# Performance work log

Hardware: AMD Instinct MI355X
Metric: run time of the kernel (lower is better)

The kernel has to match this reference:

```python
import jax, jax.numpy as jnp
import numpy as np

AT_ID = 5       # tokenizer id of '@'
CITSEG_ID = 7   # tokenizer id of 'CITSEG'


def setup_inputs() -> dict:
    key = jax.random.key(0)
    ks = jax.random.split(key, 12)
    B, S, H = 256, 512, 768
    CIT, D, NC = 750, 1518, 6
    s = lambda n: 1.0 / np.sqrt(n)
    return {
        "tokens": jax.random.randint(ks[0], (B, S), 0, 100),
        "hidden_states": jax.random.normal(ks[1], (B, S, H), jnp.float32),
        "proj_w": jax.random.normal(ks[2], (H, CIT), jnp.float32) * s(H),
        "proj_b": jax.random.normal(ks[3], (CIT,), jnp.float32) * 0.02,
        "enc_w": jax.random.normal(ks[4], (CIT, CIT), jnp.float32) * s(CIT),
        "enc_b": jax.random.normal(ks[5], (CIT,), jnp.float32) * 0.02,
        "w1": jax.random.normal(ks[6], (D, 2 * D), jnp.float32) * s(D),
        "b1": jax.random.normal(ks[7], (2 * D,), jnp.float32) * 0.02,
        "w2": jax.random.normal(ks[8], (2 * D, 2 * D), jnp.float32) * s(2 * D),
        "b2": jax.random.normal(ks[9], (2 * D,), jnp.float32) * 0.02,
        "w3": jax.random.normal(ks[10], (2 * D, NC), jnp.float32) * s(2 * D),
        "b3": jax.random.normal(ks[11], (NC,), jnp.float32) * 0.02,
    }


def _forward(tokens, hidden_states, proj_w, proj_b, enc_w, enc_b,
             w1, b1, w2, b2, w3, b3):
    B, S, H = hidden_states.shape
    idx = jnp.arange(S)[None, :]                       # [1,S]
    BIG = S + 1

    # --- ctx_pooler: masked max over tokens outside the [start,end] '@' span ---
    at_mask = tokens == AT_ID                          # [B,S]
    first = jnp.min(jnp.where(at_mask, idx, BIG), axis=1)            # [B]
    second = jnp.min(jnp.where(at_mask & (idx > first[:, None]), idx, BIG), axis=1)
    ge2 = at_mask.sum(axis=1) >= 2
    start = jnp.where(ge2, first, 0)
    end = jnp.where(ge2, second, S)                    # end=S excludes everything
    keep = (idx < start[:, None]) | (idx > end[:, None])             # [B,S]
    neg = jnp.finfo(hidden_states.dtype).min
    pooled = jnp.max(jnp.where(keep[:, :, None], hidden_states, neg), axis=1)  # [B,H]
    pooled = jnp.where(keep.any(axis=1)[:, None], pooled, 0.0)

    # --- CITSEG token gather + projection (zero row if absent) ---
    c_mask = tokens == CITSEG_ID
    c_first = jnp.min(jnp.where(c_mask, idx, BIG), axis=1)           # [B]
    has_c = c_mask.any(axis=1)
    safe_pos = jnp.minimum(c_first, S - 1)
    cit_h = jnp.take_along_axis(hidden_states, safe_pos[:, None, None], axis=1)[:, 0]  # [B,H]
    cit = (cit_h @ proj_w + proj_b) * has_c[:, None].astype(hidden_states.dtype)       # [B,750]

    # --- citseg_encoder (modeled as Linear 750->750) ---
    cit_enc = cit @ enc_w + enc_b

    # --- MLP head ---
    x = jnp.concatenate([pooled, cit_enc], axis=1)     # [B,1518]
    x = jax.nn.relu(x @ w1 + b1)
    x = jax.nn.relu(x @ w2 + b2)
    return x @ w3 + b3                                 # [B,num_class]


def reference(tokens, hidden_states, proj_w, proj_b, enc_w, enc_b,
              w1, b1, w2, b2, w3, b3):
    return _forward(tokens, hidden_states, proj_w, proj_b, enc_w, enc_b,
                    w1, b1, w2, b2, w3, b3)
```

## Files before the change

### kernel.cpp

```cpp
#include <hip/hip_runtime.h>
#include <hip/hip_bf16.h>

typedef __attribute__((ext_vector_type(8))) short bf16x8;
typedef __attribute__((ext_vector_type(4))) float f32x4;
typedef __attribute__((ext_vector_type(4))) unsigned short u16x4;

#define NEGINF (-3.4028234663852886e38f)

__device__ __forceinline__ unsigned short f2b(float f) {
    union { float f; unsigned u; } x; x.f = f;
    unsigned r = x.u + 0x7FFFu + ((x.u >> 16) & 1u);
    return (unsigned short)(r >> 16);
}
__device__ __forceinline__ float b2f(unsigned short b) {
    union { unsigned u; float f; } x; x.u = ((unsigned)b) << 16;
    return x.f;
}

__device__ __forceinline__ void load_lds16(const void* g, void* l) {
    __builtin_amdgcn_global_load_lds((const __attribute__((address_space(1))) void*)g,
                                     (__attribute__((address_space(3))) void*)l, 16, 0, 0);
}

__device__ __forceinline__ void trans32(const float* __restrict__ in, int K, int N,
                                        unsigned short* __restrict__ out, int ldo,
                                        int bx, int by, int tid, float (*tile)[33]) {
    int n0 = bx * 32, k0 = by * 32;
    int tx = tid & 31, ty = tid >> 5;
#pragma unroll
    for (int i = 0; i < 4; ++i) {
        int k = k0 + ty * 4 + i, n = n0 + tx;
        tile[ty * 4 + i][tx] = (k < K && n < N) ? in[(size_t)k * N + n] : 0.f;
    }
    __syncthreads();
    int n = tid >> 3, kc = tid & 7;
    u16x4 o;
#pragma unroll
    for (int q = 0; q < 4; ++q) o[q] = f2b(tile[kc * 4 + q][n]);
    *(u16x4*)(out + (size_t)(n0 + n) * ldo + k0 + kc * 4) = o;
}

__global__ __launch_bounds__(256) void prep_k(
    const int* __restrict__ tokens, int* __restrict__ meta,
    const float* __restrict__ proj_w, const float* __restrict__ enc_w,
    const float* __restrict__ w1, const float* __restrict__ w2,
    unsigned short* __restrict__ projT, unsigned short* __restrict__ encT,
    unsigned short* __restrict__ w1T, unsigned short* __restrict__ w2T) {
    __shared__ float tile[32][33];
    int bid = blockIdx.x, tid = threadIdx.x;
    if (bid < 64) {
        const int S = 512, BIG = 1 << 20;
        int b = bid * 4 + (tid >> 6), l = tid & 63;
        const int* row = tokens + (size_t)b * S;
        int base = l * 8;
        int toks[8];
#pragma unroll
        for (int i = 0; i < 8; ++i) toks[i] = row[base + i];
        int am = 0, cnt = 0, minAt = BIG, minC = BIG;
#pragma unroll
        for (int i = 0; i < 8; ++i) {
            if (toks[i] == 5) { am |= 1 << i; cnt++; if (base + i < minAt) minAt = base + i; }
            if (toks[i] == 7) { if (base + i < minC) minC = base + i; }
        }
        for (int off = 1; off < 64; off <<= 1) {
            minAt = min(minAt, __shfl_xor(minAt, off));
            minC  = min(minC,  __shfl_xor(minC,  off));
            cnt  += __shfl_xor(cnt, off);
        }
        int first = minAt, minAt2 = BIG;
#pragma unroll
        for (int i = 0; i < 8; ++i)
            if ((am >> i) & 1) { int idx = base + i; if (idx > first && idx < minAt2) minAt2 = idx; }
        for (int off = 1; off < 64; off <<= 1) minAt2 = min(minAt2, __shfl_xor(minAt2, off));
        if (l == 0) {
            int ge2 = (cnt >= 2) ? 1 : 0;
            int start = ge2 ? first : 0;
            int end = ge2 ? minAt2 : S;
            int anyKeep = (ge2 && (start > 0 || end < S - 1)) ? 1 : 0;
            int has_c = (minC < S) ? 1 : 0;
            int cpos = min(minC, S - 1);
            int* m = meta + b * 6;
            m[0] = start; m[1] = end; m[2] = cpos; m[3] = has_c; m[4] = anyKeep; m[5] = 0;
        }
    } else if (bid < 640) {
        int r = bid - 64;   trans32(proj_w, 768, 750, projT, 768, r % 24, r / 24, tid, tile);
    } else if (bid < 1216) {
        int r = bid - 640;  trans32(enc_w, 750, 750, encT, 768, r % 24, r / 24, tid, tile);
    } else if (bid < 5824) {
        int r = bid - 1216; trans32(w1, 1518, 3036, w1T, 1536, r % 96, r / 96, tid, tile);
    } else {
        int r = bid - 5824; trans32(w2, 3036, 3036, w2T, 3072, r % 96, r / 96, tid, tile);
    }
}

__global__ __launch_bounds__(192) void pool_k(const float* __restrict__ hs,
                                              const int* __restrict__ meta,
                                              float* __restrict__ part) {
    int b = blockIdx.x >> 3, ch = blockIdx.x & 7;
    int start = meta[b * 6 + 0], end = meta[b * 6 + 1];
    int t = threadIdx.x;
    f32x4 m = { NEGINF, NEGINF, NEGINF, NEGINF };
    const float* basep = hs + (size_t)b * 512 * 768 + t * 4;
    int s0 = ch * 64, hi = s0 + 64;
    int e1 = min(start, hi);
    int s2 = max(end + 1, s0);
#pragma unroll 4
    for (int s = s0; s < e1; ++s) {
        f32x4 v = *(const f32x4*)(basep + (size_t)s * 768);
#pragma unroll
        for (int j = 0; j < 4; ++j) m[j] = fmaxf(m[j], v[j]);
    }
#pragma unroll 4
    for (int s = s2; s < hi; ++s) {
        f32x4 v = *(const f32x4*)(basep + (size_t)s * 768);
#pragma unroll
        for (int j = 0; j < 4; ++j) m[j] = fmaxf(m[j], v[j]);
    }
    *(f32x4*)(part + ((size_t)b * 8 + ch) * 768 + t * 4) = m;
}

__global__ __launch_bounds__(192) void pack_k(const float* __restrict__ hs,
                                              const float* __restrict__ part,
                                              const int* __restrict__ meta,
                                              unsigned short* __restrict__ xA,
                                              unsigned short* __restrict__ citA) {
    int b = blockIdx.x, t = threadIdx.x;
    const float* p = part + (size_t)b * 8 * 768 + t * 4;
    f32x4 m = *(const f32x4*)p;
#pragma unroll
    for (int ch = 1; ch < 8; ++ch) {
        f32x4 v = *(const f32x4*)(p + (size_t)ch * 768);
#pragma unroll
        for (int j = 0; j < 4; ++j) m[j] = fmaxf(m[j], v[j]);
    }
    if (!meta[b * 6 + 4]) {
        f32x4 z = {0.f, 0.f, 0.f, 0.f};
        m = z;
    }
    u16x4 o;
#pragma unroll
    for (int j = 0; j < 4; ++j) o[j] = f2b(m[j]);
    *(u16x4*)(xA + (size_t)b * 1536 + t * 4) = o;

    int cpos = meta[b * 6 + 2];
    f32x4 c = *(const f32x4*)(hs + ((size_t)b * 512 + cpos) * 768 + t * 4);
    u16x4 co;
#pragma unroll
    for (int j = 0; j < 4; ++j) co[j] = f2b(c[j]);
    *(u16x4*)(citA + (size_t)b * 768 + t * 4) = co;
}

template<int EPI>
__global__ __launch_bounds__(256, 2) void gemm_k(
    const unsigned short* __restrict__ A, int lda,
    const unsigned short* __restrict__ Bt, int ldb,
    const float* __restrict__ bias, const int* __restrict__ meta,
    unsigned short* __restrict__ X, int ldx, int Nreal, int Kp) {
    __shared__ __align__(16) unsigned short As[2][64 * 128];
    __shared__ __align__(16) unsigned short Bs[2][64 * 128];
    const int tid = threadIdx.x;
    const int wid = tid >> 6, lane = tid & 63;
    const int m0 = blockIdx.y * 64, n0 = blockIdx.x * 64;
    const int wr = wid >> 1, wc = wid & 1;
    const int c_lin = lane & 15;
    const int rsub = lane >> 4;

    int aoff[4], boff[4], ldst[4];
#pragma unroll
    for (int i = 0; i < 4; ++i) {
        int r = wid * 16 + i * 4 + rsub;
        int csrc = (c_lin ^ (r & 15)) << 3;
        aoff[i] = (m0 + r) * lda + csrc;
        boff[i] = (n0 + r) * ldb + csrc;
        ldst[i] = (wid * 16 + i * 4) * 128;
    }
    int cswz[4];
#pragma unroll
    for (int ks = 0; ks < 4; ++ks) cswz[ks] = ((ks * 4 + (lane >> 4)) ^ c_lin) << 3;
    int arow[2], brow[2];
#pragma unroll
    for (int mi = 0; mi < 2; ++mi) arow[mi] = (wr * 32 + mi * 16 + c_lin) * 128;
#pragma unroll
    for (int nj = 0; nj < 2; ++nj) brow[nj] = (wc * 32 + nj * 16 + c_lin) * 128;

    f32x4 acc[2][2];
    const f32x4 zero = {0.f, 0.f, 0.f, 0.f};
#pragma unroll
    for (int mi = 0; mi < 2; ++mi)
#pragma unroll
        for (int nj = 0; nj < 2; ++nj) acc[mi][nj] = zero;

    auto stage = [&](int nb, int kt) {
#pragma unroll
        for (int i = 0; i < 4; ++i) load_lds16(A + aoff[i] + kt, &As[nb][ldst[i]]);
#pragma unroll
        for (int i = 0; i < 4; ++i) load_lds16(Bt + boff[i] + kt, &Bs[nb][ldst[i]]);
    };

    const int nt = Kp >> 7;
    stage(0, 0);
    int cb = 0;
    for (int t = 0; t < nt; ++t) {
        __syncthreads();
        if (t + 1 < nt) stage(cb ^ 1, (t + 1) << 7);
        const unsigned short* as = As[cb];
        const unsigned short* bs = Bs[cb];
#pragma unroll
        for (int ks = 0; ks < 4; ++ks) {
            bf16x8 af[2], bfr[2];
#pragma unroll
            for (int mi = 0; mi < 2; ++mi) af[mi] = *(const bf16x8*)(as + arow[mi] + cswz[ks]);
#pragma unroll
            for (int nj = 0; nj < 2; ++nj) bfr[nj] = *(const bf16x8*)(bs + brow[nj] + cswz[ks]);
#pragma unroll
            for (int mi = 0; mi < 2; ++mi)
#pragma unroll
                for (int nj = 0; nj < 2; ++nj)
                    acc[mi][nj] = __builtin_amdgcn_mfma_f32_16x16x32_bf16(
                        af[mi], bfr[nj], acc[mi][nj], 0, 0, 0);
        }
        cb ^= 1;
    }
#pragma unroll
    for (int mi = 0; mi < 2; ++mi) {
        int rowb = m0 + wr * 32 + mi * 16 + (lane >> 4) * 4;
#pragma unroll
        for (int nj = 0; nj < 2; ++nj) {
            int col = n0 + wc * 32 + nj * 16 + (lane & 15);
            float bv = (col < Nreal) ? bias[col] : 0.f;
#pragma unroll
            for (int i = 0; i < 4; ++i) {
                int row = rowb + i;
                float v = acc[mi][nj][i] + bv;
                if (EPI == 0) v *= (meta[row * 6 + 3] ? 1.f : 0.f);
                if (EPI == 2) v = fmaxf(v, 0.f);
                if (col >= Nreal) v = 0.f;
                X[(size_t)row * ldx + col] = f2b(v);
            }
        }
    }
}

__global__ __launch_bounds__(256) void out_k(const unsigned short* __restrict__ x2,
                                             const float* __restrict__ w3,
                                             const float* __restrict__ b3,
                                             float* __restrict__ out) {
    int b = blockIdx.x, t = threadIdx.x;
    int wid = t >> 6, lane = t & 63;
    float s[6] = {0.f, 0.f, 0.f, 0.f, 0.f, 0.f};
    const unsigned short* xr = x2 + (size_t)b * 3072;
    for (int k = t; k < 3036; k += 256) {
        float x = b2f(xr[k]);
#pragma unroll
        for (int j = 0; j < 6; ++j) s[j] += x * w3[(size_t)k * 6 + j];
    }
#pragma unroll
    for (int j = 0; j < 6; ++j)
        for (int off = 1; off < 64; off <<= 1) s[j] += __shfl_xor(s[j], off);
    __shared__ float red[4][6];
    if (lane == 0) {
#pragma unroll
        for (int j = 0; j < 6; ++j) red[wid][j] = s[j];
    }
    __syncthreads();
    if (t < 6) out[b * 6 + t] = red[0][t] + red[1][t] + red[2][t] + red[3][t] + b3[t];
}

extern "C" void kernel_launch(void* const* d_in, const int* in_sizes, int n_in,
                              void* d_out, int out_size, void* d_ws, size_t ws_size,
                              hipStream_t stream) {
    const int*   tokens = (const int*)d_in[0];
    const float* hs     = (const float*)d_in[1];
    const float* proj_w = (const float*)d_in[2];
    const float* proj_b = (const float*)d_in[3];
    const float* enc_w  = (const float*)d_in[4];
    const float* enc_b  = (const float*)d_in[5];
    const float* w1 = (const float*)d_in[6];
    const float* b1 = (const float*)d_in[7];
    const float* w2 = (const float*)d_in[8];
    const float* b2 = (const float*)d_in[9];
    const float* w3 = (const float*)d_in[10];
    const float* b3 = (const float*)d_in[11];
    float* out = (float*)d_out;

    char* ws = (char*)d_ws;
    size_t off = 0;
    auto alloc = [&](size_t bytes) {
        void* p = ws + off;
        off = (off + bytes + 255) & ~(size_t)255;
        return p;
    };
    int* meta            = (int*)alloc(256 * 6 * sizeof(int));
    float* part          = (float*)alloc((size_t)256 * 8 * 768 * sizeof(float));
    unsigned short* xA   = (unsigned short*)alloc((size_t)256 * 1536 * 2);
    unsigned short* citA = (unsigned short*)alloc((size_t)256 * 768 * 2);
    unsigned short* citB = (unsigned short*)alloc((size_t)256 * 768 * 2);
    unsigned short* x1   = (unsigned short*)alloc((size_t)256 * 3072 * 2);
    unsigned short* x2   = (unsigned short*)alloc((size_t)256 * 3072 * 2);
    unsigned short* projT= (unsigned short*)alloc((size_t)768 * 768 * 2);
    unsigned short* encT = (unsigned short*)alloc((size_t)768 * 768 * 2);
    unsigned short* w1T  = (unsigned short*)alloc((size_t)3072 * 1536 * 2);
    unsigned short* w2T  = (unsigned short*)alloc((size_t)3072 * 3072 * 2);

    prep_k<<<15040, 256, 0, stream>>>(tokens, meta, proj_w, enc_w, w1, w2,
                                      projT, encT, w1T, w2T);
    pool_k<<<2048, 192, 0, stream>>>(hs, meta, part);
    pack_k<<<256, 192, 0, stream>>>(hs, part, meta, xA, citA);

    gemm_k<0><<<dim3(12, 4), 256, 0, stream>>>(citA, 768, projT, 768, proj_b, meta,
                                               citB, 768, 750, 768);
    gemm_k<1><<<dim3(12, 4), 256, 0, stream>>>(citB, 768, encT, 768, enc_b, meta,
                                               xA + 768, 1536, 750, 768);
    gemm_k<2><<<dim3(48, 4), 256, 0, stream>>>(xA, 1536, w1T, 1536, b1, meta,
                                               x1, 3072, 3036, 1536);
    gemm_k<2><<<dim3(48, 4), 256, 0, stream>>>(x1, 3072, w2T, 3072, b2, meta,
                                               x2, 3072, 3036, 3072);
    out_k<<<256, 256, 0, stream>>>(x2, w3, b3, out);
}
```

Baseline: 165.9 us.

## Fuse pooling with weight transposes and pack with first GEMM into fewer launches

```diff
diff --git a/kernel.cpp b/kernel.cpp
--- a/kernel.cpp
+++ b/kernel.cpp
@@ -16,41 +16,20 @@
     union { unsigned u; float f; } x; x.u = ((unsigned)b) << 16;
     return x.f;
 }
-
 __device__ __forceinline__ void load_lds16(const void* g, void* l) {
     __builtin_amdgcn_global_load_lds((const __attribute__((address_space(1))) void*)g,
                                      (__attribute__((address_space(3))) void*)l, 16, 0, 0);
 }
 
-__device__ __forceinline__ void trans32(const float* __restrict__ in, int K, int N,
-                                        unsigned short* __restrict__ out, int ldo,
-                                        int bx, int by, int tid, float (*tile)[33]) {
-    int n0 = bx * 32, k0 = by * 32;
-    int tx = tid & 31, ty = tid >> 5;
-#pragma unroll
-    for (int i = 0; i < 4; ++i) {
-        int k = k0 + ty * 4 + i, n = n0 + tx;
-        tile[ty * 4 + i][tx] = (k < K && n < N) ? in[(size_t)k * N + n] : 0.f;
-    }
-    __syncthreads();
-    int n = tid >> 3, kc = tid & 7;
-    u16x4 o;
-#pragma unroll
-    for (int q = 0; q < 4; ++q) o[q] = f2b(tile[kc * 4 + q][n]);
-    *(u16x4*)(out + (size_t)(n0 + n) * ldo + k0 + kc * 4) = o;
-}
-
-__global__ __launch_bounds__(256) void prep_k(
-    const int* __restrict__ tokens, int* __restrict__ meta,
-    const float* __restrict__ proj_w, const float* __restrict__ enc_w,
-    const float* __restrict__ w1, const float* __restrict__ w2,
-    unsigned short* __restrict__ projT, unsigned short* __restrict__ encT,
-    unsigned short* __restrict__ w1T, unsigned short* __restrict__ w2T) {
-    __shared__ float tile[32][33];
-    int bid = blockIdx.x, tid = threadIdx.x;
-    if (bid < 64) {
-        const int S = 512, BIG = 1 << 20;
-        int b = bid * 4 + (tid >> 6), l = tid & 63;
+__global__ __launch_bounds__(192) void scan_cit_k(const int* __restrict__ tokens,
+                                                  const float* __restrict__ hs,
+                                                  int* __restrict__ meta,
+                                                  unsigned short* __restrict__ citA) {
+    __shared__ int sm;
+    const int S = 512, BIG = 1 << 20;
+    int b = blockIdx.x, tid = threadIdx.x;
+    if (tid < 64) {
+        int l = tid;
         const int* row = tokens + (size_t)b * S;
         int base = l * 8;
         int toks[8];
@@ -81,73 +60,201 @@
             int cpos = min(minC, S - 1);
             int* m = meta + b * 6;
             m[0] = start; m[1] = end; m[2] = cpos; m[3] = has_c; m[4] = anyKeep; m[5] = 0;
-        }
-    } else if (bid < 640) {
-        int r = bid - 64;   trans32(proj_w, 768, 750, projT, 768, r % 24, r / 24, tid, tile);
-    } else if (bid < 1216) {
-        int r = bid - 640;  trans32(enc_w, 750, 750, encT, 768, r % 24, r / 24, tid, tile);
-    } else if (bid < 5824) {
-        int r = bid - 1216; trans32(w1, 1518, 3036, w1T, 1536, r % 96, r / 96, tid, tile);
-    } else {
-        int r = bid - 5824; trans32(w2, 3036, 3036, w2T, 3072, r % 96, r / 96, tid, tile);
-    }
-}
-
-__global__ __launch_bounds__(192) void pool_k(const float* __restrict__ hs,
-                                              const int* __restrict__ meta,
-                                              float* __restrict__ part) {
-    int b = blockIdx.x >> 3, ch = blockIdx.x & 7;
-    int start = meta[b * 6 + 0], end = meta[b * 6 + 1];
-    int t = threadIdx.x;
-    f32x4 m = { NEGINF, NEGINF, NEGINF, NEGINF };
-    const float* basep = hs + (size_t)b * 512 * 768 + t * 4;
-    int s0 = ch * 64, hi = s0 + 64;
-    int e1 = min(start, hi);
-    int s2 = max(end + 1, s0);
+            sm = cpos;
+        }
+    }
+    __syncthreads();
+    int cpos = sm;
+    f32x4 c = *(const f32x4*)(hs + ((size_t)b * 512 + cpos) * 768 + tid * 4);
+    u16x4 co;
+#pragma unroll
+    for (int j = 0; j < 4; ++j) co[j] = f2b(c[j]);
+    *(u16x4*)(citA + (size_t)b * 768 + tid * 4) = co;
+}
+
+__device__ __forceinline__ void trans32(const float* __restrict__ in, int K, int N,
+                                        unsigned short* __restrict__ out, int ldo,
+                                        int bx, int by, int tid, float (*tile)[33]) {
+    int n0 = bx * 32, k0 = by * 32;
+    int tx = tid & 31, ty = tid >> 5;
+#pragma unroll
+    for (int i = 0; i < 4; ++i) {
+        int k = k0 + ty * 4 + i, n = n0 + tx;
+        tile[ty * 4 + i][tx] = (k < K && n < N) ? in[(size_t)k * N + n] : 0.f;
+    }
+    __syncthreads();
+    int n = tid >> 3, kc = tid & 7;
+    u16x4 o;
+#pragma unroll
+    for (int q = 0; q < 4; ++q) o[q] = f2b(tile[kc * 4 + q][n]);
+    *(u16x4*)(out + (size_t)(n0 + n) * ldo + k0 + kc * 4) = o;
+}
+
+__global__ __launch_bounds__(256) void pool_trans_k(
+    const float* __restrict__ hs, const int* __restrict__ meta,
+    float* __restrict__ part,
+    const float* __restrict__ proj_w, const float* __restrict__ enc_w,
+    const float* __restrict__ w1, const float* __restrict__ w2,
+    unsigned short* __restrict__ projT, unsigned short* __restrict__ encT,
+    unsigned short* __restrict__ w1T, unsigned short* __restrict__ w2T) {
+    __shared__ float tile[32][33];
+    int bid = blockIdx.x, tid = threadIdx.x;
+    if (bid < 2048) {
+        if (tid >= 192) return;
+        int b = bid >> 3, ch = bid & 7;
+        int start = meta[b * 6 + 0], end = meta[b * 6 + 1];
+        f32x4 m = { NEGINF, NEGINF, NEGINF, NEGINF };
+        const float* basep = hs + (size_t)b * 512 * 768 + tid * 4;
+        int s0 = ch * 64, hi = s0 + 64;
+        int e1 = min(start, hi);
+        int s2 = max(end + 1, s0);
 #pragma unroll 4
-    for (int s = s0; s < e1; ++s) {
-        f32x4 v = *(const f32x4*)(basep + (size_t)s * 768);
-#pragma unroll
-        for (int j = 0; j < 4; ++j) m[j] = fmaxf(m[j], v[j]);
-    }
+        for (int s = s0; s < e1; ++s) {
+            f32x4 v = *(const f32x4*)(basep + (size_t)s * 768);
+#pragma unroll
+            for (int j = 0; j < 4; ++j) m[j] = fmaxf(m[j], v[j]);
+        }
 #pragma unroll 4
-    for (int s = s2; s < hi; ++s) {
-        f32x4 v = *(const f32x4*)(basep + (size_t)s * 768);
-#pragma unroll
-        for (int j = 0; j < 4; ++j) m[j] = fmaxf(m[j], v[j]);
-    }
-    *(f32x4*)(part + ((size_t)b * 8 + ch) * 768 + t * 4) = m;
-}
-
-__global__ __launch_bounds__(192) void pack_k(const float* __restrict__ hs,
-                                              const float* __restrict__ part,
-                                              const int* __restrict__ meta,
-                                              unsigned short* __restrict__ xA,
-                                              unsigned short* __restrict__ citA) {
-    int b = blockIdx.x, t = threadIdx.x;
-    const float* p = part + (size_t)b * 8 * 768 + t * 4;
-    f32x4 m = *(const f32x4*)p;
-#pragma unroll
-    for (int ch = 1; ch < 8; ++ch) {
-        f32x4 v = *(const f32x4*)(p + (size_t)ch * 768);
-#pragma unroll
-        for (int j = 0; j < 4; ++j) m[j] = fmaxf(m[j], v[j]);
-    }
-    if (!meta[b * 6 + 4]) {
-        f32x4 z = {0.f, 0.f, 0.f, 0.f};
-        m = z;
-    }
-    u16x4 o;
-#pragma unroll
-    for (int j = 0; j < 4; ++j) o[j] = f2b(m[j]);
-    *(u16x4*)(xA + (size_t)b * 1536 + t * 4) = o;
-
-    int cpos = meta[b * 6 + 2];
-    f32x4 c = *(const f32x4*)(hs + ((size_t)b * 512 + cpos) * 768 + t * 4);
-    u16x4 co;
-#pragma unroll
-    for (int j = 0; j < 4; ++j) co[j] = f2b(c[j]);
-    *(u16x4*)(citA + (size_t)b * 768 + t * 4) = co;
+        for (int s = s2; s < hi; ++s) {
+            f32x4 v = *(const f32x4*)(basep + (size_t)s * 768);
+#pragma unroll
+            for (int j = 0; j < 4; ++j) m[j] = fmaxf(m[j], v[j]);
+        }
+        *(f32x4*)(part + ((size_t)b * 8 + ch) * 768 + tid * 4) = m;
+        return;
+    }
+    int r = bid - 2048;
+    if (r < 576)       { trans32(proj_w, 768, 750, projT, 768, r % 24, r / 24, tid, tile); return; }
+    r -= 576;
+    if (r < 576)       { trans32(enc_w, 750, 750, encT, 768, r % 24, r / 24, tid, tile); return; }
+    r -= 576;
+    if (r < 4608)      { trans32(w1, 1518, 3036, w1T, 1536, r % 96, r / 96, tid, tile); return; }
+    r -= 4608;
+    trans32(w2, 3036, 3036, w2T, 3072, r % 96, r / 96, tid, tile);
+}
+
+template<int EPI>
+__device__ __forceinline__ void gemm_body(
+    const unsigned short* __restrict__ A, int lda,
+    const unsigned short* __restrict__ Bt, int ldb,
+    const float* __restrict__ bias, const int* __restrict__ meta,
+    unsigned short* __restrict__ X, int ldx, int Nreal, int Kp,
+    int bx, int by, unsigned short* AsB, unsigned short* BsB) {
+    const int tid = threadIdx.x;
+    const int wid = tid >> 6, lane = tid & 63;
+    const int m0 = by * 64, n0 = bx * 64;
+    const int wr = wid >> 1, wc = wid & 1;
+    const int c_lin = lane & 15;
+    const int rsub = lane >> 4;
+
+    int aoff[4], boff[4], ldst[4];
+#pragma unroll
+    for (int i = 0; i < 4; ++i) {
+        int r = wid * 16 + i * 4 + rsub;
+        int csrc = (c_lin ^ (r & 15)) << 3;
+        aoff[i] = (m0 + r) * lda + csrc;
+        boff[i] = (n0 + r) * ldb + csrc;
+        ldst[i] = (wid * 16 + i * 4) * 128;
+    }
+    int cswz[4];
+#pragma unroll
+    for (int ks = 0; ks < 4; ++ks) cswz[ks] = ((ks * 4 + (lane >> 4)) ^ c_lin) << 3;
+    int arow[2], brow[2];
+#pragma unroll
+    for (int mi = 0; mi < 2; ++mi) arow[mi] = (wr * 32 + mi * 16 + c_lin) * 128;
+#pragma unroll
+    for (int nj = 0; nj < 2; ++nj) brow[nj] = (wc * 32 + nj * 16 + c_lin) * 128;
+
+    f32x4 acc[2][2];
+    const f32x4 zero = {0.f, 0.f, 0.f, 0.f};
+#pragma unroll
+    for (int mi = 0; mi < 2; ++mi)
+#pragma unroll
+        for (int nj = 0; nj < 2; ++nj) acc[mi][nj] = zero;
+
+    auto stage = [&](int nb, int kt) {
+#pragma unroll
+        for (int i = 0; i < 4; ++i) load_lds16(A + aoff[i] + kt, AsB + nb * 8192 + ldst[i]);
+#pragma unroll
+        for (int i = 0; i < 4; ++i) load_lds16(Bt + boff[i] + kt, BsB + nb * 8192 + ldst[i]);
+    };
+
+    const int nt = Kp >> 7;
+    stage(0, 0);
+    int cb = 0;
+    for (int t = 0; t < nt; ++t) {
+        __syncthreads();
+        if (t + 1 < nt) stage(cb ^ 1, (t + 1) << 7);
+        const unsigned short* as = AsB + cb * 8192;
+        const unsigned short* bs = BsB + cb * 8192;
+#pragma unroll
+        for (int ks = 0; ks < 4; ++ks) {
+            bf16x8 af[2], bfr[2];
+#pragma unroll
+            for (int mi = 0; mi < 2; ++mi) af[mi] = *(const bf16x8*)(as + arow[mi] + cswz[ks]);
+#pragma unroll
+            for (int nj = 0; nj < 2; ++nj) bfr[nj] = *(const bf16x8*)(bs + brow[nj] + cswz[ks]);
+#pragma unroll
+            for (int mi = 0; mi < 2; ++mi)
+#pragma unroll
+                for (int nj = 0; nj < 2; ++nj)
+                    acc[mi][nj] = __builtin_amdgcn_mfma_f32_16x16x32_bf16(
+                        af[mi], bfr[nj], acc[mi][nj], 0, 0, 0);
+        }
+        cb ^= 1;
+    }
+#pragma unroll
+    for (int mi = 0; mi < 2; ++mi) {
+        int rowb = m0 + wr * 32 + mi * 16 + (lane >> 4) * 4;
+#pragma unroll
+        for (int nj = 0; nj < 2; ++nj) {
+            int col = n0 + wc * 32 + nj * 16 + (lane & 15);
+            float bv = (col < Nreal) ? bias[col] : 0.f;
+#pragma unroll
+            for (int i = 0; i < 4; ++i) {
+                int row = rowb + i;
+                float v = acc[mi][nj][i] + bv;
+                if (EPI == 0) v *= (meta[row * 6 + 3] ? 1.f : 0.f);
+                if (EPI == 2) v = fmaxf(v, 0.f);
+                if (col >= Nreal) v = 0.f;
+                X[(size_t)row * ldx + col] = f2b(v);
+            }
+        }
+    }
+}
+
+__global__ __launch_bounds__(256, 2) void pack_g1_k(
+    const float* __restrict__ part, const int* __restrict__ meta,
+    unsigned short* __restrict__ xA,
+    const unsigned short* __restrict__ citA, const unsigned short* __restrict__ projT,
+    const float* __restrict__ proj_b, unsigned short* __restrict__ citB) {
+    __shared__ __align__(16) unsigned short As[2][64 * 128];
+    __shared__ __align__(16) unsigned short Bs[2][64 * 128];
+    int bid = blockIdx.x, tid = threadIdx.x;
+    if (bid < 256) {
+        if (tid >= 192) return;
+        int b = bid;
+        const float* p = part + (size_t)b * 8 * 768 + tid * 4;
+        f32x4 m = *(const f32x4*)p;
+#pragma unroll
+        for (int ch = 1; ch < 8; ++ch) {
+            f32x4 v = *(const f32x4*)(p + (size_t)ch * 768);
+#pragma unroll
+            for (int j = 0; j < 4; ++j) m[j] = fmaxf(m[j], v[j]);
+        }
+        if (!meta[b * 6 + 4]) {
+            f32x4 z = {0.f, 0.f, 0.f, 0.f};
+            m = z;
+        }
+        u16x4 o;
+#pragma unroll
+        for (int j = 0; j < 4; ++j) o[j] = f2b(m[j]);
+        *(u16x4*)(xA + (size_t)b * 1536 + tid * 4) = o;
+        return;
+    }
+    int r = bid - 256;
+    gemm_body<0>(citA, 768, projT, 768, proj_b, meta, citB, 768, 750, 768,
+                 r % 12, r / 12, &As[0][0], &Bs[0][0]);
 }
 
 template<int EPI>
@@ -158,87 +265,8 @@
     unsigned short* __restrict__ X, int ldx, int Nreal, int Kp) {
     __shared__ __align__(16) unsigned short As[2][64 * 128];
     __shared__ __align__(16) unsigned short Bs[2][64 * 128];
-    const int tid = threadIdx.x;
-    const int wid = tid >> 6, lane = tid & 63;
-    const int m0 = blockIdx.y * 64, n0 = blockIdx.x * 64;
-    const int wr = wid >> 1, wc = wid & 1;
-    const int c_lin = lane & 15;
-    const int rsub = lane >> 4;
-
-    int aoff[4], boff[4], ldst[4];
-#pragma unroll
-    for (int i = 0; i < 4; ++i) {
-        int r = wid * 16 + i * 4 + rsub;
-        int csrc = (c_lin ^ (r & 15)) << 3;
-        aoff[i] = (m0 + r) * lda + csrc;
-        boff[i] = (n0 + r) * ldb + csrc;
-        ldst[i] = (wid * 16 + i * 4) * 128;
-    }
-    int cswz[4];
-#pragma unroll
-    for (int ks = 0; ks < 4; ++ks) cswz[ks] = ((ks * 4 + (lane >> 4)) ^ c_lin) << 3;
-    int arow[2], brow[2];
-#pragma unroll
-    for (int mi = 0; mi < 2; ++mi) arow[mi] = (wr * 32 + mi * 16 + c_lin) * 128;
-#pragma unroll
-    for (int nj = 0; nj < 2; ++nj) brow[nj] = (wc * 32 + nj * 16 + c_lin) * 128;
-
-    f32x4 acc[2][2];
-    const f32x4 zero = {0.f, 0.f, 0.f, 0.f};
-#pragma unroll
-    for (int mi = 0; mi < 2; ++mi)
-#pragma unroll
-        for (int nj = 0; nj < 2; ++nj) acc[mi][nj] = zero;
-
-    auto stage = [&](int nb, int kt) {
-#pragma unroll
-        for (int i = 0; i < 4; ++i) load_lds16(A + aoff[i] + kt, &As[nb][ldst[i]]);
-#pragma unroll
-        for (int i = 0; i < 4; ++i) load_lds16(Bt + boff[i] + kt, &Bs[nb][ldst[i]]);
-    };
-
-    const int nt = Kp >> 7;
-    stage(0, 0);
-    int cb = 0;
-    for (int t = 0; t < nt; ++t) {
-        __syncthreads();
-        if (t + 1 < nt) stage(cb ^ 1, (t + 1) << 7);
-        const unsigned short* as = As[cb];
-        const unsigned short* bs = Bs[cb];
-#pragma unroll
-        for (int ks = 0; ks < 4; ++ks) {
-            bf16x8 af[2], bfr[2];
-#pragma unroll
-            for (int mi = 0; mi < 2; ++mi) af[mi] = *(const bf16x8*)(as + arow[mi] + cswz[ks]);
-#pragma unroll
-            for (int nj = 0; nj < 2; ++nj) bfr[nj] = *(const bf16x8*)(bs + brow[nj] + cswz[ks]);
-#pragma unroll
-            for (int mi = 0; mi < 2; ++mi)
-#pragma unroll
-                for (int nj = 0; nj < 2; ++nj)
-                    acc[mi][nj] = __builtin_amdgcn_mfma_f32_16x16x32_bf16(
-                        af[mi], bfr[nj], acc[mi][nj], 0, 0, 0);
-        }
-        cb ^= 1;
-    }
-#pragma unroll
-    for (int mi = 0; mi < 2; ++mi) {
-        int rowb = m0 + wr * 32 + mi * 16 + (lane >> 4) * 4;
-#pragma unroll
-        for (int nj = 0; nj < 2; ++nj) {
-            int col = n0 + wc * 32 + nj * 16 + (lane & 15);
-            float bv = (col < Nreal) ? bias[col] : 0.f;
-#pragma unroll
-            for (int i = 0; i < 4; ++i) {
-                int row = rowb + i;
-                float v = acc[mi][nj][i] + bv;
-                if (EPI == 0) v *= (meta[row * 6 + 3] ? 1.f : 0.f);
-                if (EPI == 2) v = fmaxf(v, 0.f);
-                if (col >= Nreal) v = 0.f;
-                X[(size_t)row * ldx + col] = f2b(v);
-            }
-        }
-    }
+    gemm_body<EPI>(A, lda, Bt, ldb, bias, meta, X, ldx, Nreal, Kp,
+                   blockIdx.x, blockIdx.y, &As[0][0], &Bs[0][0]);
 }
 
 __global__ __launch_bounds__(256) void out_k(const unsigned short* __restrict__ x2,
@@ -302,13 +330,10 @@
     unsigned short* w1T  = (unsigned short*)alloc((size_t)3072 * 1536 * 2);
     unsigned short* w2T  = (unsigned short*)alloc((size_t)3072 * 3072 * 2);
 
-    prep_k<<<15040, 256, 0, stream>>>(tokens, meta, proj_w, enc_w, w1, w2,
-                                      projT, encT, w1T, w2T);
-    pool_k<<<2048, 192, 0, stream>>>(hs, meta, part);
-    pack_k<<<256, 192, 0, stream>>>(hs, part, meta, xA, citA);
-
-    gemm_k<0><<<dim3(12, 4), 256, 0, stream>>>(citA, 768, projT, 768, proj_b, meta,
-                                               citB, 768, 750, 768);
+    scan_cit_k<<<256, 192, 0, stream>>>(tokens, hs, meta, citA);
+    pool_trans_k<<<2048 + 576 + 576 + 4608 + 9216, 256, 0, stream>>>(
+        hs, meta, part, proj_w, enc_w, w1, w2, projT, encT, w1T, w2T);
+    pack_g1_k<<<304, 256, 0, stream>>>(part, meta, xA, citA, projT, proj_b, citB);
     gemm_k<1><<<dim3(12, 4), 256, 0, stream>>>(citB, 768, encT, 768, enc_b, meta,
                                                xA + 768, 1536, 750, 768);
     gemm_k<2><<<dim3(48, 4), 256, 0, stream>>>(xA, 1536, w1T, 1536, b1, meta,
```

After: 153.2 us. 7.7% less time.
